# Kernel optimization log

Hardware: AMD Instinct MI355X
Metric: run time of the kernel (lower is better)

## Reference

```python
import jax, jax.numpy as jnp
import numpy as np

S = 3072      # total tokens across all images
DIM = 1280    # hidden_size
H = 16        # num_heads
HD = DIM // H # head_dim = 80
NSEG = 6      # number of images (cu_seqlens has NSEG+1 entries)


def _rotate_half(x):
    x1, x2 = jnp.split(x, 2, axis=-1)
    return jnp.concatenate([-x2, x1], axis=-1)


def setup_inputs() -> dict:
    key = jax.random.key(0)
    ks = jax.random.split(key, 12)
    hidden_states = jax.random.normal(ks[0], (S, DIM), jnp.float32)
    # realistic vision rotary embedding: half-dim inv_freq, repeated to head_dim
    inv_freq = 1.0 / (10000.0 ** (jnp.arange(0, HD // 2, dtype=jnp.float32) / (HD // 2)))
    freqs = jnp.arange(S, dtype=jnp.float32)[:, None] * inv_freq[None, :]  # [S, HD/2]
    emb = jnp.concatenate([freqs, freqs], axis=-1)  # [S, HD]
    cos = jnp.cos(emb)
    sin = jnp.sin(emb)
    sc = 0.02
    wq = jax.random.normal(ks[1], (DIM, DIM), jnp.float32) * sc
    bq = jax.random.normal(ks[2], (DIM,), jnp.float32) * sc
    wk = jax.random.normal(ks[3], (DIM, DIM), jnp.float32) * sc
    bk = jax.random.normal(ks[4], (DIM,), jnp.float32) * sc
    wv = jax.random.normal(ks[5], (DIM, DIM), jnp.float32) * sc
    bv = jax.random.normal(ks[6], (DIM,), jnp.float32) * sc
    wo = jax.random.normal(ks[7], (DIM, DIM), jnp.float32) * sc
    bo = jax.random.normal(ks[8], (DIM,), jnp.float32) * sc
    cu_seqlens = (jnp.arange(NSEG + 1, dtype=jnp.int32) * (S // NSEG))  # [0,512,...,3072]
    return dict(hidden_states=hidden_states, cos=cos, sin=sin,
                wq=wq, bq=bq, wk=wk, bk=bk, wv=wv, bv=bv, wo=wo, bo=bo,
                cu_seqlens=cu_seqlens)


def reference(hidden_states, cos, sin, wq, bq, wk, bk, wv, bv, wo, bo, cu_seqlens):
    seq_length = hidden_states.shape[0]
    scaling = HD ** (-0.5)
    # QKV projections (torch Linear: x @ W.T + b)
    q = (hidden_states @ wq.T + bq).reshape(seq_length, H, HD)
    k = (hidden_states @ wk.T + bk).reshape(seq_length, H, HD)
    v = (hidden_states @ wv.T + bv).reshape(seq_length, H, HD)
    # apply_rotary_pos_emb_vision: cos/sin [S, HD] broadcast over head axis
    c = cos[:, None, :]
    s = sin[:, None, :]
    q = q * c + _rotate_half(q) * s
    k = k * c + _rotate_half(k) * s
    # block-diagonal (per-image) attention via segment mask
    seg = jnp.searchsorted(cu_seqlens[1:], jnp.arange(seq_length), side='right')
    mask = seg[:, None] == seg[None, :]  # [S, S] bool
    scores = jnp.einsum('shd,thd->hst', q, k) * scaling  # [H, S, S]
    scores = jnp.where(mask[None, :, :], scores, jnp.finfo(scores.dtype).min)
    attn = jax.nn.softmax(scores, axis=-1)
    out = jnp.einsum('hst,thd->shd', attn, v).reshape(seq_length, DIM)
    return out @ wo.T + bo
```

## Files before the change

### kernel.cpp

```cpp
#include <hip/hip_runtime.h>
#include <hip/hip_bf16.h>
#include <hip/hip_fp16.h>
#include <cstdint>
#include <cstddef>

typedef _Float16 f16;
typedef f16 f16x2 __attribute__((ext_vector_type(2)));
typedef f16 f16x4 __attribute__((ext_vector_type(4)));
typedef f16 f16x8 __attribute__((ext_vector_type(8)));
typedef float f32x4 __attribute__((ext_vector_type(4)));

#define S_LEN 3072
#define DIM 1280
#define NH 16
#define HD 80
#define SEG 512

#define MFMA16F(a, b, c) __builtin_amdgcn_mfma_f32_16x16x32_f16((a), (b), (c), 0, 0, 0)

__device__ __forceinline__ void gl2lds16(const void* g, void* l) {
    __builtin_amdgcn_global_load_lds(
        (const __attribute__((address_space(1))) unsigned int*)g,
        (__attribute__((address_space(3))) unsigned int*)l, 16, 0, 0);
}

__device__ __forceinline__ unsigned int pack2(float a, float b) {
    f16x2 t = {(f16)a, (f16)b};
    union { f16x2 v; unsigned int u; } c;
    c.v = t;
    return c.u;
}

__global__ __launch_bounds__(256) void cvt_kernel(
    const float* __restrict__ hs,
    const float* __restrict__ wq, const float* __restrict__ wk,
    const float* __restrict__ wv, const float* __restrict__ wo,
    f16* __restrict__ hs16,
    f16* __restrict__ wq16, f16* __restrict__ wk16,
    f16* __restrict__ wv16, f16* __restrict__ wo16)
{
    const int m = blockIdx.y;
    const float* src; f16* dst; int n4;
    if (m == 0)      { src = hs; dst = hs16; n4 = S_LEN * DIM / 4; }
    else if (m == 1) { src = wq; dst = wq16; n4 = DIM * DIM / 4; }
    else if (m == 2) { src = wk; dst = wk16; n4 = DIM * DIM / 4; }
    else if (m == 3) { src = wv; dst = wv16; n4 = DIM * DIM / 4; }
    else             { src = wo; dst = wo16; n4 = DIM * DIM / 4; }
    int idx = blockIdx.x * 256 + threadIdx.x;
    if (idx >= n4) return;
    f32x4 v = *(const f32x4*)(src + (size_t)idx * 4);
    f16x4 o;
#pragma unroll
    for (int e = 0; e < 4; ++e) o[e] = (f16)v[e];
    *(f16x4*)(dst + (size_t)idx * 4) = o;
}

__global__ __launch_bounds__(512, 2) void gemm_qkv192(
    const f16* __restrict__ A, const f16* __restrict__ Wb,
    const float* __restrict__ bq, const float* __restrict__ bk,
    const float* __restrict__ bv,
    f16* __restrict__ q16, f16* __restrict__ k16, f16* __restrict__ vT)
{
    const int bid = blockIdx.x;
    const int xcd = bid & 7;
    const int idx = bid >> 3;
    const int mt = xcd * 2 + idx / 15;
    const int nt = idx % 15;
    const int m0 = mt * 192;
    const int n0 = nt * 256;

    __shared__ __align__(16) f16 Abuf[2][192 * 64];
    __shared__ __align__(16) f16 Bbuf[2][256 * 64];

    const int tid = threadIdx.x;
    const int w = tid >> 6;
    const int lane = tid & 63;
    const int lane15 = lane & 15;
    const int quad = lane >> 4;
    const int wm = (w >> 2) * 96;
    const int wn = (w & 3) * 64;

    const int srow = lane >> 3;
    const int schk = (lane & 7) ^ srow;

    const int aRow = w * 24;
    const int bRow = (w & 3) * 64 + (w >> 2) * 16;

    const f16* gA = A + (size_t)(m0 + aRow + srow) * DIM + schk * 8;
    const f16* gB = Wb + (size_t)(n0 + bRow + srow) * DIM + schk * 8;

    const int x7 = lane15 & 7;
    const int cc0 = (quad ^ x7) * 8;
    const int cc1 = ((quad + 4) ^ x7) * 8;

    f32x4 acc[6][4];
#pragma unroll
    for (int i = 0; i < 6; ++i)
#pragma unroll
        for (int j = 0; j < 4; ++j)
            acc[i][j] = (f32x4){0.f, 0.f, 0.f, 0.f};

    {
        f16* lB = Bbuf[0] + bRow * 64;
        gl2lds16(gB, lB);
        gl2lds16(gB + 8 * DIM, lB + 512);
        gl2lds16(gB + 32 * DIM, lB + 2048);
        gl2lds16(gB + 40 * DIM, lB + 2560);
        f16* lA = Abuf[0] + aRow * 64;
        gl2lds16(gA, lA);
        gl2lds16(gA + 8 * DIM, lA + 512);
        gl2lds16(gA + 16 * DIM, lA + 1024);
        f16* lB1 = Bbuf[1] + bRow * 64;
        gl2lds16(gB + 64, lB1);
        gl2lds16(gB + 8 * DIM + 64, lB1 + 512);
        gl2lds16(gB + 32 * DIM + 64, lB1 + 2048);
        gl2lds16(gB + 40 * DIM + 64, lB1 + 2560);
        f16* lA1 = Abuf[1] + aRow * 64;
        gl2lds16(gA + 64, lA1);
        gl2lds16(gA + 8 * DIM + 64, lA1 + 512);
        gl2lds16(gA + 16 * DIM + 64, lA1 + 1024);
    }
    asm volatile("s_waitcnt vmcnt(7)" ::: "memory");
    __builtin_amdgcn_s_barrier();

    f16x8 a0[3][2], a1[3][2], b01[2][2], b23[2][2];
#pragma unroll
    for (int i = 0; i < 3; ++i) {
        const f16* rp = Abuf[0] + (wm + i * 16 + lane15) * 64;
        a0[i][0] = *(const f16x8*)(rp + cc0);
        a0[i][1] = *(const f16x8*)(rp + cc1);
    }
#pragma unroll
    for (int j = 0; j < 2; ++j) {
        const f16* rp = Bbuf[0] + (wn + j * 16 + lane15) * 64;
        b01[j][0] = *(const f16x8*)(rp + cc0);
        b01[j][1] = *(const f16x8*)(rp + cc1);
    }

    for (int kt = 0; kt < 20; ++kt) {
        const int s = kt & 1;
        const int sn = s ^ 1;
        const int k2 = (kt + 2 < 20) ? kt + 2 : 19;
        const f16* As = Abuf[s];
        const f16* Bsl = Bbuf[s];
        const f16* Asn = Abuf[sn];
        const f16* Bsn = Bbuf[sn];
        const f16* gA2 = gA + k2 * 64;
        const f16* gB2 = gB + k2 * 64;

        __builtin_amdgcn_s_barrier();
        asm volatile("s_waitcnt lgkmcnt(0)" ::: "memory");
        __builtin_amdgcn_sched_barrier(0);
        __builtin_amdgcn_s_setprio(1);
#pragma unroll
        for (int i = 0; i < 3; ++i)
#pragma unroll
            for (int j = 0; j < 2; ++j) {
                acc[i][j] = MFMA16F(a0[i][0], b01[j][0], acc[i][j]);
                acc[i][j] = MFMA16F(a0[i][1], b01[j][1], acc[i][j]);
            }
        __builtin_amdgcn_s_setprio(0);
        __builtin_amdgcn_sched_barrier(0);
#pragma unroll
        for (int j = 0; j < 2; ++j) {
            const f16* rp = Bsl + (wn + 32 + j * 16 + lane15) * 64;
            b23[j][0] = *(const f16x8*)(rp + cc0);
            b23[j][1] = *(const f16x8*)(rp + cc1);
        }

        __builtin_amdgcn_s_barrier();
        asm volatile("s_waitcnt lgkmcnt(0)" ::: "memory");
        __builtin_amdgcn_sched_barrier(0);
        __builtin_amdgcn_s_setprio(1);
#pragma unroll
        for (int i = 0; i < 3; ++i)
#pragma unroll
            for (int j = 0; j < 2; ++j) {
                acc[i][j + 2] = MFMA16F(a0[i][0], b23[j][0], acc[i][j + 2]);
                acc[i][j + 2] = MFMA16F(a0[i][1], b23[j][1], acc[i][j + 2]);
            }
        __builtin_amdgcn_s_setprio(0);
        __builtin_amdgcn_sched_barrier(0);
#pragma unroll
        for (int i = 0; i < 3; ++i) {
            const f16* rp = As + (wm + 48 + i * 16 + lane15) * 64;
            a1[i][0] = *(const f16x8*)(rp + cc0);
            a1[i][1] = *(const f16x8*)(rp + cc1);
        }
        {
            f16* lB = Bbuf[s] + bRow * 64;
            gl2lds16(gB2, lB);
            gl2lds16(gB2 + 8 * DIM, lB + 512);
            gl2lds16(gB2 + 32 * DIM, lB + 2048);
            gl2lds16(gB2 + 40 * DIM, lB + 2560);
        }
        asm volatile("s_waitcnt vmcnt(4)" ::: "memory");

        __builtin_amdgcn_s_barrier();
        asm volatile("s_waitcnt lgkmcnt(0)" ::: "memory");
        __builtin_amdgcn_sched_barrier(0);
        __builtin_amdgcn_s_setprio(1);
#pragma unroll
        for (int i = 0; i < 3; ++i)
#pragma unroll
            for (int j = 0; j < 2; ++j) {
                acc[i + 3][j + 2] = MFMA16F(a1[i][0], b23[j][0], acc[i + 3][j + 2]);
                acc[i + 3][j + 2] = MFMA16F(a1[i][1], b23[j][1], acc[i + 3][j + 2]);
            }
        __builtin_amdgcn_s_setprio(0);
        __builtin_amdgcn_sched_barrier(0);
#pragma unroll
        for (int i = 0; i < 3; ++i) {
            const f16* rp = Asn + (wm + i * 16 + lane15) * 64;
            a0[i][0] = *(const f16x8*)(rp + cc0);
            a0[i][1] = *(const f16x8*)(rp + cc1);
        }
        {
            f16* lA = Abuf[s] + aRow * 64;
            gl2lds16(gA2, lA);
            gl2lds16(gA2 + 8 * DIM, lA + 512);
            gl2lds16(gA2 + 16 * DIM, lA + 1024);
        }

        __builtin_amdgcn_s_barrier();
        asm volatile("s_waitcnt lgkmcnt(0)" ::: "memory");
        __builtin_amdgcn_sched_barrier(0);
        __builtin_amdgcn_s_setprio(1);
#pragma unroll
        for (int i = 0; i < 3; ++i)
#pragma unroll
            for (int j = 0; j < 2; ++j) {
                acc[i + 3][j] = MFMA16F(a1[i][0], b01[j][0], acc[i + 3][j]);
                acc[i + 3][j] = MFMA16F(a1[i][1], b01[j][1], acc[i + 3][j]);
            }
        __builtin_amdgcn_s_setprio(0);
        __builtin_amdgcn_sched_barrier(0);
#pragma unroll
        for (int j = 0; j < 2; ++j) {
            const f16* rp = Bsn + (wn + j * 16 + lane15) * 64;
            b01[j][0] = *(const f16x8*)(rp + cc0);
            b01[j][1] = *(const f16x8*)(rp + cc1);
        }
    }
    asm volatile("s_waitcnt vmcnt(0) lgkmcnt(0)" ::: "memory");

    const int sel = nt / 5;
    const int nc0 = (nt % 5) * 256 + wn;
    const float* bias = (sel == 0) ? bq : (sel == 1) ? bk : bv;
    float bvv[4];
#pragma unroll
    for (int j = 0; j < 4; ++j) bvv[j] = bias[nc0 + j * 16 + lane15];

    if (sel < 2) {
        f16* O = sel ? k16 : q16;
#pragma unroll
        for (int i = 0; i < 6; ++i)
#pragma unroll
            for (int j = 0; j < 4; ++j)
#pragma unroll
                for (int r = 0; r < 4; ++r) {
                    int row = m0 + wm + i * 16 + quad * 4 + r;
                    O[(size_t)row * DIM + nc0 + j * 16 + lane15] =
                        (f16)(acc[i][j][r] + bvv[j]);
                }
    } else {
#pragma unroll
        for (int i = 0; i < 6; ++i)
#pragma unroll
            for (int j = 0; j < 4; ++j) {
                f16x4 ov;
#pragma unroll
                for (int r = 0; r < 4; ++r) ov[r] = (f16)(acc[i][j][r] + bvv[j]);
                int row = m0 + wm + i * 16 + quad * 4;
                int col = nc0 + j * 16 + lane15;
                *(f16x4*)(vT + (size_t)col * S_LEN + row) = ov;
            }
    }
}

__global__ __launch_bounds__(256) void gemm_out_kernel(
    const f16* __restrict__ A, const f16* __restrict__ W,
    const float* __restrict__ bias, float* __restrict__ OF)
{
    const int f = blockIdx.x;
    const int xcd = f & 7;
    const int idx = f >> 3;
    const int xt = xcd * 6 + idx % 6;
    const int yt = idx / 6;

    __shared__ __align__(16) f16 As[64 * 32];
    __shared__ __align__(16) f16 Bs[128 * 32];

    const int tid = threadIdx.x;
    const int lane = tid & 63;
    const int lane15 = tid & 15;
    const int quad = lane >> 4;
    const int w = tid >> 6;
    const int wn = w * 32;
    const int m0 = xt * 64;
    const int n0 = yt * 128;

    const int srA = w * 16 + (lane >> 2);
    const int srB = w * 32 + (lane >> 2);
    const int scol = (lane & 3) * 8;
    const f16* gA0 = A + (size_t)(m0 + srA) * DIM + scol;
    const f16* gB0 = W + (size_t)(n0 + srB) * DIM + scol;
    const f16* gB1 = W + (size_t)(n0 + srB + 16) * DIM + scol;
    f16* lA0 = As + (w * 16) * 32;
    f16* lB0 = Bs + (w * 32) * 32;
    f16* lB1 = Bs + (w * 32 + 16) * 32;

    f32x4 acc[4][2];
#pragma unroll
    for (int i = 0; i < 4; ++i)
#pragma unroll
        for (int j = 0; j < 2; ++j)
            acc[i][j] = (f32x4){0.f, 0.f, 0.f, 0.f};

    for (int kt = 0; kt < DIM / 32; ++kt) {
        __syncthreads();
        gl2lds16(gA0 + kt * 32, lA0);
        gl2lds16(gB0 + kt * 32, lB0);
        gl2lds16(gB1 + kt * 32, lB1);
        __syncthreads();

        f16x8 fa[4], fb[2];
#pragma unroll
        for (int i = 0; i < 4; ++i)
            fa[i] = *(const f16x8*)(As + (i * 16 + lane15) * 32 + quad * 8);
#pragma unroll
        for (int j = 0; j < 2; ++j)
            fb[j] = *(const f16x8*)(Bs + (wn + j * 16 + lane15) * 32 + quad * 8);
#pragma unroll
        for (int i = 0; i < 4; ++i)
#pragma unroll
            for (int j = 0; j < 2; ++j)
                acc[i][j] = MFMA16F(fa[i], fb[j], acc[i][j]);
    }

    float bvv[2];
#pragma unroll
    for (int j = 0; j < 2; ++j)
        bvv[j] = bias[n0 + wn + j * 16 + lane15];

#pragma unroll
    for (int i = 0; i < 4; ++i)
#pragma unroll
        for (int j = 0; j < 2; ++j)
#pragma unroll
            for (int r = 0; r < 4; ++r) {
                int row = m0 + i * 16 + quad * 4 + r;
                int col = n0 + wn + j * 16 + lane15;
                OF[(size_t)row * DIM + col] = acc[i][j][r] + bvv[j];
            }
}

__global__ __launch_bounds__(256) void rope_kernel(
    f16* __restrict__ qb, f16* __restrict__ kb,
    const float* __restrict__ cosb, const float* __restrict__ sinb)
{
    int idx = blockIdx.x * 256 + threadIdx.x;
    int c = idx % 5;
    int t = idx / 5;
    int h = t & 15; t >>= 4;
    int s = t % S_LEN;
    int which = t / S_LEN;
    f16* buf = which ? kb : qb;
    float scale = which ? 1.0f : 0.11180339887498948f;
    int j = c * 8;
    f32x4 ca = *(const f32x4*)(cosb + s * HD + j);
    f32x4 cb = *(const f32x4*)(cosb + s * HD + j + 4);
    f32x4 sna = *(const f32x4*)(sinb + s * HD + j);
    f32x4 snb = *(const f32x4*)(sinb + s * HD + j + 4);
    size_t base = (size_t)s * DIM + h * HD + j;
    f16x8 x1 = *(f16x8*)(buf + base);
    f16x8 x2 = *(f16x8*)(buf + base + 40);
    f16x8 o1, o2;
#pragma unroll
    for (int e = 0; e < 8; ++e) {
        float ce = (e < 4) ? ca[e] : cb[e - 4];
        float se = (e < 4) ? sna[e] : snb[e - 4];
        float a = (float)x1[e], b = (float)x2[e];
        o1[e] = (f16)((a * ce - b * se) * scale);
        o2[e] = (f16)((b * ce + a * se) * scale);
    }
    *(f16x8*)(buf + base) = o1;
    *(f16x8*)(buf + base + 40) = o2;
}

__global__ __launch_bounds__(256, 4) void attn_kernel(
    const f16* __restrict__ q, const f16* __restrict__ k,
    const f16* __restrict__ vT, f16* __restrict__ o)
{
    const int h = blockIdx.x;
    const int g = blockIdx.y;
    const int qc = blockIdx.z;
    const int tid = threadIdx.x;
    const int lane15 = tid & 15;
    const int quad = (tid & 63) >> 4;
    const int w = tid >> 6;
    const int qbase = g * SEG + qc * 64;
    const int qrow = qbase + w * 16 + lane15;

    __shared__ __align__(16) f16 Ks2[10 * 128 * 8];
    __shared__ __align__(16) f16 Vt[80 * 128];

    f16x8 zf;
#pragma unroll
    for (int e = 0; e < 8; ++e) zf[e] = (f16)0.0f;

    f16x8 fq[3];
#pragma unroll
    for (int kc = 0; kc < 3; ++kc) {
        if (kc == 2 && quad >= 2) fq[kc] = zf;
        else fq[kc] = *(const f16x8*)(q + (size_t)qrow * DIM + h * HD + kc * 32 + quad * 8);
    }

    float m_run = -1e30f, l_run = 0.f;
    f32x4 Oa[5];
#pragma unroll
    for (int dt = 0; dt < 5; ++dt) Oa[dt] = (f32x4){0.f, 0.f, 0.f, 0.f};

    for (int kt = 0; kt < 4; ++kt) {
        __syncthreads();
        const int kb = g * SEG + kt * 128;
#pragma unroll
        for (int c = tid; c < 1280; c += 256) {
            int r = c / 10;
            int ch = c - r * 10;
            int rr = r ^ (ch & 7);
            *(f16x8*)(Ks2 + ch * 1024 + rr * 8) =
                *(const f16x8*)(k + (size_t)(kb + r) * DIM + h * HD + ch * 8);
        }
#pragma unroll
        for (int c = tid; c < 1280; c += 256) {
            int d = c >> 4;
            int sc = c & 15;
            *(f16x8*)(Vt + d * 128 + (sc ^ (d & 7)) * 8) =
                *(const f16x8*)(vT + (size_t)(h * HD + d) * S_LEN + kb + sc * 8);
        }
        __syncthreads();

        f32x4 sa[8];
#pragma unroll
        for (int nt = 0; nt < 8; ++nt) sa[nt] = (f32x4){0.f, 0.f, 0.f, 0.f};
#pragma unroll
        for (int kc = 0; kc < 3; ++kc) {
#pragma unroll
            for (int nt = 0; nt < 8; ++nt) {
                f16x8 fk;
                if (kc == 2 && quad >= 2) fk = zf;
                else {
                    int ch = kc * 4 + quad;
                    int rr = (nt * 16 + lane15) ^ (ch & 7);
                    fk = *(const f16x8*)(Ks2 + ch * 1024 + rr * 8);
                }
                sa[nt] = MFMA16F(fk, fq[kc], sa[nt]);
            }
        }

        float mt = -1e30f;
#pragma unroll
        for (int nt = 0; nt < 8; ++nt)
#pragma unroll
            for (int r = 0; r < 4; ++r) mt = fmaxf(mt, sa[nt][r]);
        mt = fmaxf(mt, __shfl_xor(mt, 16, 64));
        mt = fmaxf(mt, __shfl_xor(mt, 32, 64));

        float mn = fmaxf(m_run, mt);
        float alpha = __expf(m_run - mn);
        m_run = mn;
        float lt = 0.f;
        unsigned int pp[8][2];
#pragma unroll
        for (int nt = 0; nt < 8; ++nt) {
            float p0 = __expf(sa[nt][0] - mn);
            float p1 = __expf(sa[nt][1] - mn);
            float p2 = __expf(sa[nt][2] - mn);
            float p3 = __expf(sa[nt][3] - mn);
            lt += (p0 + p1) + (p2 + p3);
            pp[nt][0] = pack2(p0, p1);
            pp[nt][1] = pack2(p2, p3);
        }
        lt += __shfl_xor(lt, 16, 64);
        lt += __shfl_xor(lt, 32, 64);
        l_run = l_run * alpha + lt;

#pragma unroll
        for (int dt = 0; dt < 5; ++dt)
#pragma unroll
            for (int r = 0; r < 4; ++r) Oa[dt][r] *= alpha;

        const int srcA = ((quad & 1) * 2) * 16 + lane15;
        const int srcB = srcA + 16;
        const bool hi = quad >= 2;
#pragma unroll
        for (int kc2 = 0; kc2 < 4; ++kc2) {
            unsigned int e0 = __shfl((int)pp[2 * kc2][0], srcA, 64);
            unsigned int e1 = __shfl((int)pp[2 * kc2][1], srcA, 64);
            unsigned int e2 = __shfl((int)pp[2 * kc2][0], srcB, 64);
            unsigned int e3 = __shfl((int)pp[2 * kc2][1], srcB, 64);
            unsigned int o0 = __shfl((int)pp[2 * kc2 + 1][0], srcA, 64);
            unsigned int o1 = __shfl((int)pp[2 * kc2 + 1][1], srcA, 64);
            unsigned int o2 = __shfl((int)pp[2 * kc2 + 1][0], srcB, 64);
            unsigned int o3 = __shfl((int)pp[2 * kc2 + 1][1], srcB, 64);
            union { unsigned int u[4]; f16x8 v; } fp;
            fp.u[0] = hi ? o0 : e0;
            fp.u[1] = hi ? o1 : e1;
            fp.u[2] = hi ? o2 : e2;
            fp.u[3] = hi ? o3 : e3;
#pragma unroll
            for (int dt = 0; dt < 5; ++dt) {
                int drow = dt * 16 + lane15;
                int slot = (kc2 * 4 + quad) ^ (drow & 7);
                f16x8 fv = *(const f16x8*)(Vt + drow * 128 + slot * 8);
                Oa[dt] = MFMA16F(fv, fp.v, Oa[dt]);
            }
        }
    }

    float inv = 1.0f / l_run;
#pragma unroll
    for (int dt = 0; dt < 5; ++dt) {
        f16x4 ov;
#pragma unroll
        for (int r = 0; r < 4; ++r) ov[r] = (f16)(Oa[dt][r] * inv);
        *(f16x4*)(o + (size_t)qrow * DIM + h * HD + dt * 16 + quad * 4) = ov;
    }
}

extern "C" void kernel_launch(void* const* d_in, const int* in_sizes, int n_in,
                              void* d_out, int out_size, void* d_ws, size_t ws_size,
                              hipStream_t stream)
{
    const float* hs   = (const float*)d_in[0];
    const float* cosb = (const float*)d_in[1];
    const float* sinb = (const float*)d_in[2];
    const float* wq   = (const float*)d_in[3];
    const float* bq   = (const float*)d_in[4];
    const float* wk   = (const float*)d_in[5];
    const float* bk   = (const float*)d_in[6];
    const float* wv   = (const float*)d_in[7];
    const float* bv   = (const float*)d_in[8];
    const float* wo   = (const float*)d_in[9];
    const float* bo   = (const float*)d_in[10];

    const size_t SD = (size_t)S_LEN * DIM;
    const size_t WW = (size_t)DIM * DIM;
    f16* hs16 = (f16*)d_ws;
    f16* wq16 = hs16 + SD;
    f16* wk16 = wq16 + WW;
    f16* wv16 = wk16 + WW;
    f16* wo16 = wv16 + WW;
    f16* q16  = wo16 + WW;
    f16* k16  = q16 + SD;
    f16* vT16 = k16 + SD;
    f16* ao16 = vT16 + SD;
    float* outb = (float*)d_out;

    cvt_kernel<<<dim3(S_LEN * DIM / 4 / 256, 5), 256, 0, stream>>>(
        hs, wq, wk, wv, wo, hs16, wq16, wk16, wv16, wo16);
    gemm_qkv192<<<240, 512, 0, stream>>>(
        hs16, wq16, bq, bk, bv, q16, k16, vT16);
    rope_kernel<<<1920, 256, 0, stream>>>(q16, k16, cosb, sinb);
    attn_kernel<<<dim3(NH, 6, 8), 256, 0, stream>>>(q16, k16, vT16, ao16);
    gemm_out_kernel<<<480, 256, 0, stream>>>(ao16, wo16, bo, outb);
}
```

Baseline: 206.1 us.

## Rewrite output projection GEMM with 128x128 tiles, double-buffered LDS and swizzle

The output projection GEMM moves from 64x128 tiles with a single-buffered K=32 loop to 128x128 tiles over K=64 steps. The LDS is double-buffered, the LDS layout is XOR-swizzled, and async global-to-LDS loads are interleaved with MFMA phases using s_setprio and sched_barrier. The goal is to hide load latency, cut bank conflicts and raise arithmetic intensity per block. In exchange the grid drops from 480 to 240 blocks, so parallelism falls, and the hand-written waitcnt ordering makes the code fragile.

```diff
diff --git a/kernel.cpp b/kernel.cpp
--- a/kernel.cpp
+++ b/kernel.cpp
@@ -278,78 +278,208 @@
     }
 }
 
-__global__ __launch_bounds__(256) void gemm_out_kernel(
+__global__ __launch_bounds__(256, 2) void gemm_out_kernel(
     const f16* __restrict__ A, const f16* __restrict__ W,
     const float* __restrict__ bias, float* __restrict__ OF)
 {
-    const int f = blockIdx.x;
-    const int xcd = f & 7;
-    const int idx = f >> 3;
-    const int xt = xcd * 6 + idx % 6;
-    const int yt = idx / 6;
-
-    __shared__ __align__(16) f16 As[64 * 32];
-    __shared__ __align__(16) f16 Bs[128 * 32];
+    const int bid = blockIdx.x;
+    const int xcd = bid & 7;
+    const int idx = bid >> 3;
+    const int mt = xcd * 3 + idx / 10;
+    const int nt = idx % 10;
+    const int m0 = mt * 128;
+    const int n0 = nt * 128;
+
+    __shared__ __align__(16) f16 Abuf[2][128 * 64];
+    __shared__ __align__(16) f16 Bbuf[2][128 * 64];
 
     const int tid = threadIdx.x;
+    const int w = tid >> 6;
     const int lane = tid & 63;
-    const int lane15 = tid & 15;
+    const int lane15 = lane & 15;
     const int quad = lane >> 4;
-    const int w = tid >> 6;
-    const int wn = w * 32;
-    const int m0 = xt * 64;
-    const int n0 = yt * 128;
-
-    const int srA = w * 16 + (lane >> 2);
-    const int srB = w * 32 + (lane >> 2);
-    const int scol = (lane & 3) * 8;
-    const f16* gA0 = A + (size_t)(m0 + srA) * DIM + scol;
-    const f16* gB0 = W + (size_t)(n0 + srB) * DIM + scol;
-    const f16* gB1 = W + (size_t)(n0 + srB + 16) * DIM + scol;
-    f16* lA0 = As + (w * 16) * 32;
-    f16* lB0 = Bs + (w * 32) * 32;
-    f16* lB1 = Bs + (w * 32 + 16) * 32;
-
-    f32x4 acc[4][2];
+    const int wm = (w >> 1) * 64;
+    const int wn = (w & 1) * 64;
+
+    const int srow = lane >> 3;
+    const int schk = (lane & 7) ^ srow;
+
+    const int aRow = w * 32;
+    const int bRow = w * 32;
+
+    const f16* gA = A + (size_t)(m0 + aRow + srow) * DIM + schk * 8;
+    const f16* gB = W + (size_t)(n0 + bRow + srow) * DIM + schk * 8;
+
+    const int x7 = lane15 & 7;
+    const int cc0 = (quad ^ x7) * 8;
+    const int cc1 = ((quad + 4) ^ x7) * 8;
+
+    f32x4 acc[4][4];
 #pragma unroll
     for (int i = 0; i < 4; ++i)
 #pragma unroll
-        for (int j = 0; j < 2; ++j)
+        for (int j = 0; j < 4; ++j)
             acc[i][j] = (f32x4){0.f, 0.f, 0.f, 0.f};
 
-    for (int kt = 0; kt < DIM / 32; ++kt) {
-        __syncthreads();
-        gl2lds16(gA0 + kt * 32, lA0);
-        gl2lds16(gB0 + kt * 32, lB0);
-        gl2lds16(gB1 + kt * 32, lB1);
-        __syncthreads();
-
-        f16x8 fa[4], fb[2];
-#pragma unroll
-        for (int i = 0; i < 4; ++i)
-            fa[i] = *(const f16x8*)(As + (i * 16 + lane15) * 32 + quad * 8);
-#pragma unroll
-        for (int j = 0; j < 2; ++j)
-            fb[j] = *(const f16x8*)(Bs + (wn + j * 16 + lane15) * 32 + quad * 8);
-#pragma unroll
-        for (int i = 0; i < 4; ++i)
-#pragma unroll
-            for (int j = 0; j < 2; ++j)
-                acc[i][j] = MFMA16F(fa[i], fb[j], acc[i][j]);
-    }
-
-    float bvv[2];
-#pragma unroll
-    for (int j = 0; j < 2; ++j)
+    {
+        f16* lB = Bbuf[0] + bRow * 64;
+        gl2lds16(gB, lB);
+        gl2lds16(gB + 8 * DIM, lB + 512);
+        gl2lds16(gB + 16 * DIM, lB + 1024);
+        gl2lds16(gB + 24 * DIM, lB + 1536);
+        f16* lA = Abuf[0] + aRow * 64;
+        gl2lds16(gA, lA);
+        gl2lds16(gA + 8 * DIM, lA + 512);
+        gl2lds16(gA + 16 * DIM, lA + 1024);
+        gl2lds16(gA + 24 * DIM, lA + 1536);
+        f16* lB1 = Bbuf[1] + bRow * 64;
+        gl2lds16(gB + 64, lB1);
+        gl2lds16(gB + 8 * DIM + 64, lB1 + 512);
+        gl2lds16(gB + 16 * DIM + 64, lB1 + 1024);
+        gl2lds16(gB + 24 * DIM + 64, lB1 + 1536);
+        f16* lA1 = Abuf[1] + aRow * 64;
+        gl2lds16(gA + 64, lA1);
+        gl2lds16(gA + 8 * DIM + 64, lA1 + 512);
+        gl2lds16(gA + 16 * DIM + 64, lA1 + 1024);
+        gl2lds16(gA + 24 * DIM + 64, lA1 + 1536);
+    }
+    asm volatile("s_waitcnt vmcnt(8)" ::: "memory");
+    __builtin_amdgcn_s_barrier();
+
+    f16x8 a0[2][2], a1[2][2], b01[2][2], b23[2][2];
+#pragma unroll
+    for (int i = 0; i < 2; ++i) {
+        const f16* rp = Abuf[0] + (wm + i * 16 + lane15) * 64;
+        a0[i][0] = *(const f16x8*)(rp + cc0);
+        a0[i][1] = *(const f16x8*)(rp + cc1);
+    }
+#pragma unroll
+    for (int j = 0; j < 2; ++j) {
+        const f16* rp = Bbuf[0] + (wn + j * 16 + lane15) * 64;
+        b01[j][0] = *(const f16x8*)(rp + cc0);
+        b01[j][1] = *(const f16x8*)(rp + cc1);
+    }
+
+    for (int kt = 0; kt < 20; ++kt) {
+        const int s = kt & 1;
+        const int sn = s ^ 1;
+        const int k2 = (kt + 2 < 20) ? kt + 2 : 19;
+        const f16* As = Abuf[s];
+        const f16* Bsl = Bbuf[s];
+        const f16* Asn = Abuf[sn];
+        const f16* Bsn = Bbuf[sn];
+        const f16* gA2 = gA + k2 * 64;
+        const f16* gB2 = gB + k2 * 64;
+
+        __builtin_amdgcn_s_barrier();
+        asm volatile("s_waitcnt lgkmcnt(0)" ::: "memory");
+        __builtin_amdgcn_sched_barrier(0);
+        __builtin_amdgcn_s_setprio(1);
+#pragma unroll
+        for (int i = 0; i < 2; ++i)
+#pragma unroll
+            for (int j = 0; j < 2; ++j) {
+                acc[i][j] = MFMA16F(a0[i][0], b01[j][0], acc[i][j]);
+                acc[i][j] = MFMA16F(a0[i][1], b01[j][1], acc[i][j]);
+            }
+        __builtin_amdgcn_s_setprio(0);
+        __builtin_amdgcn_sched_barrier(0);
+#pragma unroll
+        for (int j = 0; j < 2; ++j) {
+            const f16* rp = Bsl + (wn + 32 + j * 16 + lane15) * 64;
+            b23[j][0] = *(const f16x8*)(rp + cc0);
+            b23[j][1] = *(const f16x8*)(rp + cc1);
+        }
+
+        __builtin_amdgcn_s_barrier();
+        asm volatile("s_waitcnt lgkmcnt(0)" ::: "memory");
+        __builtin_amdgcn_sched_barrier(0);
+        __builtin_amdgcn_s_setprio(1);
+#pragma unroll
+        for (int i = 0; i < 2; ++i)
+#pragma unroll
+            for (int j = 0; j < 2; ++j) {
+                acc[i][j + 2] = MFMA16F(a0[i][0], b23[j][0], acc[i][j + 2]);
+                acc[i][j + 2] = MFMA16F(a0[i][1], b23[j][1], acc[i][j + 2]);
+            }
+        __builtin_amdgcn_s_setprio(0);
+        __builtin_amdgcn_sched_barrier(0);
+#pragma unroll
+        for (int i = 0; i < 2; ++i) {
+            const f16* rp = As + (wm + 32 + i * 16 + lane15) * 64;
+            a1[i][0] = *(const f16x8*)(rp + cc0);
+            a1[i][1] = *(const f16x8*)(rp + cc1);
+        }
+        {
+            f16* lB = Bbuf[s] + bRow * 64;
+            gl2lds16(gB2, lB);
+            gl2lds16(gB2 + 8 * DIM, lB + 512);
+            gl2lds16(gB2 + 16 * DIM, lB + 1024);
+            gl2lds16(gB2 + 24 * DIM, lB + 1536);
+        }
+        asm volatile("s_waitcnt vmcnt(4)" ::: "memory");
+
+        __builtin_amdgcn_s_barrier();
+        asm volatile("s_waitcnt lgkmcnt(0)" ::: "memory");
+        __builtin_amdgcn_sched_barrier(0);
+        __builtin_amdgcn_s_setprio(1);
+#pragma unroll
+        for (int i = 0; i < 2; ++i)
+#pragma unroll
+            for (int j = 0; j < 2; ++j) {
+                acc[i + 2][j + 2] = MFMA16F(a1[i][0], b23[j][0], acc[i + 2][j + 2]);
+                acc[i + 2][j + 2] = MFMA16F(a1[i][1], b23[j][1], acc[i + 2][j + 2]);
+            }
+        __builtin_amdgcn_s_setprio(0);
+        __builtin_amdgcn_sched_barrier(0);
+#pragma unroll
+        for (int i = 0; i < 2; ++i) {
+            const f16* rp = Asn + (wm + i * 16 + lane15) * 64;
+            a0[i][0] = *(const f16x8*)(rp + cc0);
+            a0[i][1] = *(const f16x8*)(rp + cc1);
+        }
+        {
+            f16* lA = Abuf[s] + aRow * 64;
+            gl2lds16(gA2, lA);
+            gl2lds16(gA2 + 8 * DIM, lA + 512);
+            gl2lds16(gA2 + 16 * DIM, lA + 1024);
+            gl2lds16(gA2 + 24 * DIM, lA + 1536);
+        }
+
+        __builtin_amdgcn_s_barrier();
+        asm volatile("s_waitcnt lgkmcnt(0)" ::: "memory");
+        __builtin_amdgcn_sched_barrier(0);
+        __builtin_amdgcn_s_setprio(1);
+#pragma unroll
+        for (int i = 0; i < 2; ++i)
+#pragma unroll
+            for (int j = 0; j < 2; ++j) {
+                acc[i + 2][j] = MFMA16F(a1[i][0], b01[j][0], acc[i + 2][j]);
+                acc[i + 2][j] = MFMA16F(a1[i][1], b01[j][1], acc[i + 2][j]);
+            }
+        __builtin_amdgcn_s_setprio(0);
+        __builtin_amdgcn_sched_barrier(0);
+#pragma unroll
+        for (int j = 0; j < 2; ++j) {
+            const f16* rp = Bsn + (wn + j * 16 + lane15) * 64;
+            b01[j][0] = *(const f16x8*)(rp + cc0);
+            b01[j][1] = *(const f16x8*)(rp + cc1);
+        }
+    }
+    asm volatile("s_waitcnt vmcnt(0) lgkmcnt(0)" ::: "memory");
+
+    float bvv[4];
+#pragma unroll
+    for (int j = 0; j < 4; ++j)
         bvv[j] = bias[n0 + wn + j * 16 + lane15];
 
 #pragma unroll
     for (int i = 0; i < 4; ++i)
 #pragma unroll
-        for (int j = 0; j < 2; ++j)
+        for (int j = 0; j < 4; ++j)
 #pragma unroll
             for (int r = 0; r < 4; ++r) {
-                int row = m0 + i * 16 + quad * 4 + r;
+                int row = m0 + wm + i * 16 + quad * 4 + r;
                 int col = n0 + wn + j * 16 + lane15;
                 OF[(size_t)row * DIM + col] = acc[i][j][r] + bvv[j];
             }
@@ -564,5 +694,5 @@
         hs16, wq16, bq, bk, bv, q16, k16, vT16);
     rope_kernel<<<1920, 256, 0, stream>>>(q16, k16, cosb, sinb);
     attn_kernel<<<dim3(NH, 6, 8), 256, 0, stream>>>(q16, k16, vT16, ao16);
-    gemm_out_kernel<<<480, 256, 0, stream>>>(ao16, wo16, bo, outb);
-}
+    gemm_out_kernel<<<240, 256, 0, stream>>>(ao16, wo16, bo, outb);
+}
```

Result: no change. 204.6 us (-0.8%).
